# Kernel optimization log

Hardware: AMD Instinct MI355X
Metric: run time of the kernel (lower is better)

Reference implementation:

```python
import jax, jax.numpy as jnp
import numpy as np

DIM = 64

def conv2d_g2(x, w, b):
    # 3x3 conv, padding=1, groups=2, NCHW
    y = jax.lax.conv_general_dilated(x, w, (1, 1), [(1, 1), (1, 1)],
                                     dimension_numbers=('NCHW', 'OIHW', 'NCHW'),
                                     feature_group_count=2)
    return y + b[None, :, None, None]

def bilinear_gather(x, py, px):
    # x: [B,C,H,W]; py,px: [B,K,H,W] float sample coords -> [B,K,H,W,C]
    B, C, H, W = x.shape
    y0 = jnp.floor(py); x0 = jnp.floor(px)
    ly = py - y0; lx = px - x0
    hy = 1.0 - ly; hx = 1.0 - lx
    b_idx = jnp.arange(B)[:, None, None, None]
    def gather(yi, xi):
        valid = (yi >= 0) & (yi < H) & (xi >= 0) & (xi < W)
        yc = jnp.clip(yi, 0, H - 1).astype(jnp.int32)
        xc = jnp.clip(xi, 0, W - 1).astype(jnp.int32)
        v = x[b_idx, :, yc, xc]  # [B,K,H,W,C]
        return v * valid[..., None].astype(x.dtype)
    return (gather(y0, x0) * (hy * hx)[..., None]
            + gather(y0, x0 + 1) * (hy * lx)[..., None]
            + gather(y0 + 1, x0) * (ly * hx)[..., None]
            + gather(y0 + 1, x0 + 1) * (ly * lx)[..., None])

def deform_dw(x, offset, w, b, k, pad, dil):
    # depthwise (groups=C, offset_groups=1) deformable conv, stride 1
    B, C, H, W = x.shape
    K = k * k
    off = offset.reshape(B, K, 2, H, W)  # torchvision layout: (dy,dx) per kernel tap
    ky = jnp.repeat(jnp.arange(k), k).astype(x.dtype)   # [K]
    kx = jnp.tile(jnp.arange(k), k).astype(x.dtype)     # [K]
    base_y = jnp.arange(H, dtype=x.dtype)[None, None, :, None] - pad + dil * ky[None, :, None, None]
    base_x = jnp.arange(W, dtype=x.dtype)[None, None, None, :] - pad + dil * kx[None, :, None, None]
    py = base_y + off[:, :, 0]  # [B,K,H,W]
    px = base_x + off[:, :, 1]
    val = bilinear_gather(x, py, px)  # [B,K,H,W,C]
    return jnp.einsum('bkhwc,ck->bchw', val, w.reshape(C, K)) + b[None, :, None, None]

def lsk_forward(x, w_off3, b_off3, w_off2, b_off2, w7, b7, w5, b5):
    B, C, H, W = x.shape
    offset3 = conv2d_g2(x, w_off3, b_off3)            # [B,98,H,W]
    out1 = deform_dw(x, offset3, w7, b7, 7, 9, 3)     # [B,C,H,W]
    offset2 = conv2d_g2(x, w_off2, b_off2)            # [B,50,H,W]
    out2 = deform_dw(out1, offset2, w5, b5, 5, 6, 3)  # [B,C,H,W]
    feats = jnp.stack([out1, out2], axis=1)           # [B,2,C,H,W]
    gap = feats.mean(axis=(3, 4), keepdims=True)      # [B,2,C,1,1]
    attn = jax.nn.softmax(gap, axis=1)
    return jnp.sum(feats * attn, axis=1)              # [B,C,H,W]

def setup_inputs() -> dict:
    key = jax.random.key(0)
    ks = jax.random.split(key, 9)
    B, C, H, W = 4, DIM, 56, 56
    return {
        'x':      jax.random.normal(ks[0], (B, C, H, W), jnp.float32),
        'w_off3': jax.random.normal(ks[1], (98, C // 2, 3, 3), jnp.float32) * 0.05,
        'b_off3': jax.random.normal(ks[2], (98,), jnp.float32) * 0.05,
        'w_off2': jax.random.normal(ks[3], (50, C // 2, 3, 3), jnp.float32) * 0.05,
        'b_off2': jax.random.normal(ks[4], (50,), jnp.float32) * 0.05,
        'w7':     jax.random.normal(ks[5], (C, 1, 7, 7), jnp.float32) * 0.1,
        'b7':     jax.random.normal(ks[6], (C,), jnp.float32) * 0.05,
        'w5':     jax.random.normal(ks[7], (C, 1, 5, 5), jnp.float32) * 0.1,
        'b5':     jax.random.normal(ks[8], (C,), jnp.float32) * 0.05,
    }

def reference(x, w_off3, b_off3, w_off2, b_off2, w7, b7, w5, b5):
    return lsk_forward(x, w_off3, b_off3, w_off2, b_off2, w7, b7, w5, b5)
```

## Files before the change

kernel.cpp:

```cpp
#include <hip/hip_runtime.h>
#include <hip/hip_fp16.h>
#include <math.h>

#define HH 56
#define WW 56
#define CC 64
#define BB 4
#define HWA (HH*WW)

typedef _Float16 half8_t __attribute__((ext_vector_type(8)));
typedef _Float16 h2_t   __attribute__((ext_vector_type(2)));
typedef float f32x4_t __attribute__((ext_vector_type(4)));

#define PROWS 57
#define PSTRB (PROWS*57*64*4)
#define ROWSTRB (57*64*4)

__global__ __launch_bounds__(256)
void k_prep(const float* __restrict__ x,
            const float* __restrict__ w3, const float* __restrict__ w2,
            const float* __restrict__ b3, const float* __restrict__ b2,
            __half2* __restrict__ xp, _Float16* __restrict__ xh,
            _Float16* __restrict__ Wp, float* __restrict__ bbp) {
    int blk = blockIdx.x;
    int tid = threadIdx.x;
    if (blk < BB*56) {
        __shared__ float ld[64*57];
        int b = blk / 56, y = blk % 56;
        for (int i = tid; i < 64*56; i += 256) {
            int c = i / 56, col = i % 56;
            ld[c*57 + col] = x[((size_t)b*CC + c)*HWA + y*WW + col];
        }
        __syncthreads();
        for (int i = tid; i < 57*64; i += 256) {
            int j = i >> 6, c = i & 63;
            float lo = (j > 0)  ? ld[c*57 + j - 1] : 0.f;
            float hi = (j < 56) ? ld[c*57 + j]     : 0.f;
            xp[((size_t)(b*PROWS + y)*57 + j)*CC + c] = __floats2half2_rn(lo, hi);
        }
        _Float16* dst = xh + (((size_t)(b*2)*56 + y)*58)*32;
#pragma unroll
        for (int g = 0; g < 2; ++g) {
            for (int i = tid; i < 1856; i += 256) {
                int col = i >> 5, ic = i & 31;
                float v = (col >= 1 && col <= 56) ? ld[(g*32 + ic)*57 + col - 1] : 0.f;
                dst[(size_t)g*(56*58*32) + i] = (_Float16)v;
            }
        }
    } else {
        int i = (blk - BB*56)*256 + tid;
        if (i < 46080) {
            int j    = i & 7;
            int lane = (i >> 3) & 63;
            int mt   = (i >> 9) % 5;
            int kt   = (i / 2560) % 9;
            int g    = i / 23040;
            int m  = mt*16 + (lane & 15);
            int ic = (lane >> 4)*8 + j;
            int ky = kt/3, kx = kt%3;
            float v = 0.f;
            if (m < 49)      v = w3[((g*49 + m)*32 + ic)*9 + ky*3 + kx];
            else if (m < 74) v = w2[((g*25 + (m-49))*32 + ic)*9 + ky*3 + kx];
            Wp[i] = (_Float16)v;
        } else if (i < 46240) {
            int t = i - 46080; int g = t/80, m = t%80;
            float v = 0.f;
            if (m < 49)      v = b3[g*49 + m];
            else if (m < 74) v = b2[g*25 + (m-49)];
            bbp[t] = v;
        }
    }
}

__global__ __launch_bounds__(256)
void k_convmfma(const _Float16* __restrict__ xh, const _Float16* __restrict__ Wp,
                const float* __restrict__ bb,
                float* __restrict__ off3, float* __restrict__ off2) {
    __shared__ _Float16 tile[4][3*18*32];
    int blk = blockIdx.x;
    int iy = blk % 56;
    int g  = (blk / 56) & 1;
    int b  = blk / 112;
    int wv   = threadIdx.y;
    int lane = threadIdx.x;
    int n0 = wv * 16;

    const uint4* xs4 = (const uint4*)xh;
    uint4* tl4 = (uint4*)&tile[wv][0];
#pragma unroll
    for (int i = 0; i < 4; ++i) {
        int idx4 = i*64 + lane;
        if (idx4 < 216) {
            int ic4 = idx4 & 3;
            int seg = idx4 >> 2;
            int cl = seg % 18, r = seg / 18;
            int y = iy - 1 + r, col = n0 + cl;
            uint4 v = {0u, 0u, 0u, 0u};
            if (y >= 0 && y < 56 && col < 58)
                v = xs4[((((size_t)(b*2+g)*56 + y)*58 + col) << 2) + ic4];
            tl4[idx4] = v;
        }
    }
    __syncthreads();

    int nlo = lane & 15, khi = lane >> 4;
    f32x4_t acc[5];
#pragma unroll
    for (int mt = 0; mt < 5; ++mt) acc[mt] = (f32x4_t){0.f,0.f,0.f,0.f};

    const half8_t* wp8 = (const half8_t*)Wp;
#pragma unroll
    for (int kt = 0; kt < 9; ++kt) {
        int ky = kt/3, kx = kt%3;
        half8_t bfrag = *(const half8_t*)&tile[wv][((ky*18) + nlo + kx)*32 + khi*8];
#pragma unroll
        for (int mt = 0; mt < 5; ++mt) {
            half8_t afrag = wp8[(((size_t)g*9 + kt)*5 + mt)*64 + lane];
            acc[mt] = __builtin_amdgcn_mfma_f32_16x16x32_f16(afrag, bfrag, acc[mt], 0, 0, 0);
        }
    }

    int pixcol = n0 + nlo;
    if (pixcol < 56) {
        int pix = iy*WW + pixcol;
#pragma unroll
        for (int mt = 0; mt < 5; ++mt) {
#pragma unroll
            for (int r = 0; r < 4; ++r) {
                int m = mt*16 + khi*4 + r;
                if (m < 74) {
                    float val = acc[mt][r] + bb[g*80 + m];
                    if (m < 49)
                        off3[((size_t)b*98 + g*49 + m)*HWA + pix] = val;
                    else
                        off2[((size_t)b*50 + g*25 + (m-49))*HWA + pix] = val;
                }
            }
        }
    }
}

template<int K, int KS, int PAD, bool WP>
__global__ __launch_bounds__(256)
void k_deform(const _Float16* __restrict__ xp, const float* __restrict__ off,
              const float* __restrict__ wg, const float* __restrict__ bias,
              float* __restrict__ out, float* __restrict__ partial,
              _Float16* __restrict__ xpo) {
    __shared__ float lwf[K*64];
    __shared__ float loffs[2*K][9];
    __shared__ float red[8][64];
    int tid = threadIdx.x + threadIdx.y*64;
    int blk = blockIdx.x;
    int xcd = blk & 7;
    int idx = blk >> 3;
    int b   = xcd >> 1;
    int hw0 = (xcd & 1)*(HWA/2) + idx*8;

    for (int i = tid; i < K*64; i += 256) {
        int cch = i / K, t = i % K;
        lwf[t*64 + cch] = wg[i];
    }
    for (int i = tid; i < 4*K; i += 256) {
        int row = i >> 1, half = i & 1;
        float4 v = *(const float4*)&off[((size_t)b*2*K + row)*HWA + hw0 + half*4];
        loffs[row][half*4 + 0] = v.x; loffs[row][half*4 + 1] = v.y;
        loffs[row][half*4 + 2] = v.z; loffs[row][half*4 + 3] = v.w;
    }
    __syncthreads();

    int yp = threadIdx.y;
    int c  = threadIdx.x;

    int mx0 = 0, wz0 = 0, ww0 = 0;
    int mx1 = 0, wz1 = 0, ww1 = 0;
    if (c < K) {
        int t = c;
        int ky = t / KS, kx = t % KS;
#pragma unroll
        for (int s = 0; s < 2; ++s) {
            int p = yp + 4*s;
            int hw = hw0 + p;
            int h = hw / WW, w = hw % WW;
            float py = (float)(h - PAD + 3*ky) + loffs[2*t][p];
            float px = (float)(w - PAD + 3*kx) + loffs[2*t+1][p];
            float y0f = floorf(py), x0f = floorf(px);
            float ly = py - y0f, lx = px - x0f;
            float hy = 1.f - ly, hx = 1.f - lx;
            int y0 = (int)y0f, x0 = (int)x0f;
            int j = x0 + 1;
            bool jv = (j >= 0) && (j <= 56);
            int jc = jv ? j : 0;
            float s0 = ((y0   >= 0) && (y0   < HH) && jv) ? hy : 0.f;
            float s1 = ((y0+1 >= 0) && (y0+1 < HH) && jv) ? ly : 0.f;
            bool use1 = (s0 == 0.f);
            int rbase = use1 ? min(max(y0 + 1, 0), 55) : y0;
            float aw = use1 ? s1 : s0;
            float bw = use1 ? 0.f : s1;
            int mxv = (rbase*57 + jc)*(64*4);
            __half2 wah = __floats2half2_rn(aw*hx, aw*lx);
            __half2 wbh = __floats2half2_rn(bw*hx, bw*lx);
            if (s == 0) { mx0 = mxv; wz0 = *(int*)&wah; ww0 = *(int*)&wbh; }
            else        { mx1 = mxv; wz1 = *(int*)&wah; ww1 = *(int*)&wbh; }
        }
    }

    int grp = c >> 4, li = c & 15;
    int voffb = (grp & 1) * ROWSTRB + li * 16;
    bool pix1 = (grp & 2) != 0;
    bool rowB = (grp & 1) != 0;
    const char* xb = (const char*)xp + (size_t)b*PSTRB;

    f32x4_t acc = (f32x4_t){0.f, 0.f, 0.f, 0.f};
#pragma unroll 8
    for (int t = 0; t < K; ++t) {
        int m0 = (int)__builtin_amdgcn_readlane(mx0, t);
        int m1 = (int)__builtin_amdgcn_readlane(mx1, t);
        int z0 = (int)__builtin_amdgcn_readlane(wz0, t);
        int w0 = (int)__builtin_amdgcn_readlane(ww0, t);
        int z1 = (int)__builtin_amdgcn_readlane(wz1, t);
        int w1 = (int)__builtin_amdgcn_readlane(ww1, t);
        int msel = pix1 ? m1 : m0;
        int wsel = pix1 ? (rowB ? w1 : z1) : (rowB ? w0 : z0);
        uint4 d = *(const uint4*)(xb + msel + voffb);
        float4 lv = *(const float4*)&lwf[t*64 + 4*li];
        h2_t wh = *(h2_t*)&wsel;
        acc[0] = fmaf(__builtin_amdgcn_fdot2(*(h2_t*)&d.x, wh, 0.f, false), lv.x, acc[0]);
        acc[1] = fmaf(__builtin_amdgcn_fdot2(*(h2_t*)&d.y, wh, 0.f, false), lv.y, acc[1]);
        acc[2] = fmaf(__builtin_amdgcn_fdot2(*(h2_t*)&d.z, wh, 0.f, false), lv.z, acc[2]);
        acc[3] = fmaf(__builtin_amdgcn_fdot2(*(h2_t*)&d.w, wh, 0.f, false), lv.w, acc[3]);
    }

    float4 bs4 = *(const float4*)&bias[4*li];
    float o0 = acc[0] + __shfl_xor(acc[0], 16) + bs4.x;
    float o1 = acc[1] + __shfl_xor(acc[1], 16) + bs4.y;
    float o2 = acc[2] + __shfl_xor(acc[2], 16) + bs4.z;
    float o3 = acc[3] + __shfl_xor(acc[3], 16) + bs4.w;

    int hwA = hw0 + yp, hwB = hw0 + yp + 4;
    if (grp == 0) {
        float4 o = {o0, o1, o2, o3};
        *(float4*)&red[yp][4*li] = o;
        *(float4*)&out[((size_t)b*HWA + hwA)*CC + 4*li] = o;
    } else if (grp == 2) {
        float4 o = {o0, o1, o2, o3};
        *(float4*)&red[yp + 4][4*li] = o;
        *(float4*)&out[((size_t)b*HWA + hwB)*CC + 4*li] = o;
    }
    __syncthreads();

    if (WP) {
        float val0 = red[yp][c];
        float val1 = red[yp + 4][c];
#pragma unroll
        for (int s = 0; s < 2; ++s) {
            int hw = s ? hwB : hwA;
            float val = s ? val1 : val0;
            int y = hw / WW, w = hw % WW;
            _Float16* base = xpo + ((size_t)(b*PROWS + y)*57)*CC*2;
            _Float16 hv = (_Float16)val;
            base[((w    )*64 + c)*2 + 1] = hv;
            base[((w + 1)*64 + c)*2 + 0] = hv;
            if (w == 0)  base[(c)*2 + 0] = (_Float16)0.f;
            if (w == 55) base[((56)*64 + c)*2 + 1] = (_Float16)0.f;
        }
    }

    if (yp == 0) {
        float s = red[0][c] + red[1][c] + red[2][c] + red[3][c]
                + red[4][c] + red[5][c] + red[6][c] + red[7][c];
        partial[((size_t)b*(HWA/8) + (hw0 >> 3))*64 + c] = s;
    }
}

__global__ void k_gapA(const float* __restrict__ p1, const float* __restrict__ p2,
                       float* __restrict__ g2) {
    __shared__ float red[4][64];
    int blk = blockIdx.x;
    int chunk = blk % 14;
    int bf    = blk / 14;
    int b     = bf >> 1;
    const float* p = (bf & 1) ? p2 : p1;
    int tid = threadIdx.x;
    int c = tid & 63, s = tid >> 6;
    float sum = 0.f;
#pragma unroll
    for (int i = 0; i < 7; ++i) {
        int j = chunk*28 + s + 4*i;
        sum += p[((size_t)b*(HWA/8) + j)*64 + c];
    }
    red[s][c] = sum;
    __syncthreads();
    if (s == 0)
        g2[((size_t)bf*14 + chunk)*64 + c]
            = red[0][c] + red[1][c] + red[2][c] + red[3][c];
}

__global__ void k_combine16(const float* __restrict__ o1, const float* __restrict__ o2,
                            const float* __restrict__ g2, float* __restrict__ out) {
    __shared__ float ash[128];
    __shared__ float tile[16][65];
    int blk = blockIdx.x;
    int tid = threadIdx.x;
    int b  = blk / 196;
    int t0 = (blk % 196) * 16;

    if (tid < 64) {
        float s1 = 0.f, s2 = 0.f;
#pragma unroll
        for (int k = 0; k < 14; ++k) {
            s1 += g2[((size_t)(b*2+0)*14 + k)*64 + tid];
            s2 += g2[((size_t)(b*2+1)*14 + k)*64 + tid];
        }
        s1 *= (1.f/HWA); s2 *= (1.f/HWA);
        float m  = fmaxf(s1, s2);
        float e1 = expf(s1 - m), e2 = expf(s2 - m);
        float a1 = e1 / (e1 + e2);
        ash[tid]      = a1;
        ash[64 + tid] = 1.f - a1;
    }
    __syncthreads();

    int p  = tid >> 4, c4 = tid & 15;
    size_t idx4 = ((size_t)b*HWA + t0 + p)*16 + c4;
    float4 v1 = ((const float4*)o1)[idx4];
    float4 v2 = ((const float4*)o2)[idx4];
    tile[p][c4*4 + 0] = v1.x*ash[c4*4+0] + v2.x*ash[64+c4*4+0];
    tile[p][c4*4 + 1] = v1.y*ash[c4*4+1] + v2.y*ash[64+c4*4+1];
    tile[p][c4*4 + 2] = v1.z*ash[c4*4+2] + v2.z*ash[64+c4*4+2];
    tile[p][c4*4 + 3] = v1.w*ash[c4*4+3] + v2.w*ash[64+c4*4+3];
    __syncthreads();

    int px = tid & 15, c0 = tid >> 4;
#pragma unroll
    for (int i = 0; i < 4; ++i) {
        int c = c0 + 16*i;
        out[((size_t)b*CC + c)*HWA + t0 + px] = tile[px][c];
    }
}

extern "C" void kernel_launch(void* const* d_in, const int* in_sizes, int n_in,
                              void* d_out, int out_size, void* d_ws, size_t ws_size,
                              hipStream_t stream) {
    const float* x      = (const float*)d_in[0];
    const float* w_off3 = (const float*)d_in[1];
    const float* b_off3 = (const float*)d_in[2];
    const float* w_off2 = (const float*)d_in[3];
    const float* b_off2 = (const float*)d_in[4];
    const float* w7     = (const float*)d_in[5];
    const float* b7     = (const float*)d_in[6];
    const float* w5     = (const float*)d_in[7];
    const float* b5     = (const float*)d_in[8];
    float* out = (float*)d_out;

    const size_t PAIRF = (size_t)BB*PROWS*57*64;
    float* ws    = (float*)d_ws;
    float* off3r = ws;
    float* off2r = off3r + 1229312;
    float* out1  = off2r + 627200;
    float* out2  = out1  + 802816;
    float* xp1f  = out2  + 802816;
    float* xp2f  = xp1f  + PAIRF;
    float* xhf   = xp2f  + PAIRF;
    float* part1 = xhf   + 415744;
    float* part2 = part1 + 100352;
    float* gpA   = part2 + 100352;
    float* wpf   = gpA   + 7168;
    float* bbp   = wpf   + 23040;
    __half2*  xp1  = (__half2*)xp1f;
    _Float16* xp2h = (_Float16*)xp2f;
    _Float16* xh   = (_Float16*)xhf;
    _Float16* Wp   = (_Float16*)wpf;
    size_t need = (size_t)(1229312 + 627200 + 802816*2 + 831744*2 + 415744
                           + 100352*2 + 7168 + 23040 + 160) * 4;
    if (ws_size < need) return;

    k_prep<<<BB*56 + 181, 256, 0, stream>>>(x, w_off3, w_off2, b_off3, b_off2,
                                            xp1, xh, Wp, bbp);
    k_convmfma<<<BB*2*56, dim3(64,4), 0, stream>>>(xh, Wp, bbp, off3r, off2r);
    k_deform<49,7,9,true><<<BB*(HWA/8), dim3(64,4), 0, stream>>>(
        (const _Float16*)xp1, off3r, w7, b7, out1, part1, xp2h);
    k_deform<25,5,6,false><<<BB*(HWA/8), dim3(64,4), 0, stream>>>(
        xp2h, off2r, w5, b5, out2, part2, nullptr);
    k_gapA<<<8*14, 256, 0, stream>>>(part1, part2, gpA);
    k_combine16<<<BB*196, 256, 0, stream>>>(out1, out2, gpA, out);
}
```

Before: 143.1 us.

## Shrink deform blocks to 4 pixels, one thread per channel, atomic GAP reduction

The deform kernel now uses 128-thread blocks covering 4 pixels instead of 256-thread blocks covering 8. Each lane owns one channel and gathers half2 pairs from both rows itself, rather than splitting rows and channel quads across lane groups and combining them with a shuffle. The separate partial-sum GAP kernel is removed: each block atomically adds its channel sums into a small zeroed buffer that combine reads directly. This doubles the number of blocks and cuts launch count by one. In exchange it uses narrower 4-byte gathers, repeats per-block weight staging twice as often, and adds atomics plus a memset.

```diff
diff --git a/kernel.cpp b/kernel.cpp
--- a/kernel.cpp
+++ b/kernel.cpp
@@ -140,31 +140,27 @@
     }
 }
 
-template<int K, int KS, int PAD, bool WP>
-__global__ __launch_bounds__(256)
+template<int K, int KS, int PAD, bool WP, int FL>
+__global__ __launch_bounds__(128)
 void k_deform(const _Float16* __restrict__ xp, const float* __restrict__ off,
               const float* __restrict__ wg, const float* __restrict__ bias,
-              float* __restrict__ out, float* __restrict__ partial,
+              float* __restrict__ out, float* __restrict__ gpA2,
               _Float16* __restrict__ xpo) {
-    __shared__ float lwf[K*64];
-    __shared__ float loffs[2*K][9];
-    __shared__ float red[8][64];
+    __shared__ float lw[K*64];
+    __shared__ float loffs[2*K][4];
+    __shared__ float red[4][64];
     int tid = threadIdx.x + threadIdx.y*64;
     int blk = blockIdx.x;
     int xcd = blk & 7;
     int idx = blk >> 3;
     int b   = xcd >> 1;
-    int hw0 = (xcd & 1)*(HWA/2) + idx*8;
-
-    for (int i = tid; i < K*64; i += 256) {
-        int cch = i / K, t = i % K;
-        lwf[t*64 + cch] = wg[i];
-    }
-    for (int i = tid; i < 4*K; i += 256) {
-        int row = i >> 1, half = i & 1;
-        float4 v = *(const float4*)&off[((size_t)b*2*K + row)*HWA + hw0 + half*4];
-        loffs[row][half*4 + 0] = v.x; loffs[row][half*4 + 1] = v.y;
-        loffs[row][half*4 + 2] = v.z; loffs[row][half*4 + 3] = v.w;
+    int hw0 = (xcd & 1)*(HWA/2) + idx*4;
+
+    for (int i = tid; i < K*64; i += 128)
+        lw[i] = wg[i];
+    for (int i = tid; i < 2*K; i += 128) {
+        float4 v = *(const float4*)&off[((size_t)b*2*K + i)*HWA + hw0];
+        *(float4*)&loffs[i][0] = v;
     }
     __syncthreads();
 
@@ -178,7 +174,7 @@
         int ky = t / KS, kx = t % KS;
 #pragma unroll
         for (int s = 0; s < 2; ++s) {
-            int p = yp + 4*s;
+            int p = yp + 2*s;
             int hw = hw0 + p;
             int h = hw / WW, w = hw % WW;
             float py = (float)(h - PAD + 3*ky) + loffs[2*t][p];
@@ -204,53 +200,36 @@
         }
     }
 
-    int grp = c >> 4, li = c & 15;
-    int voffb = (grp & 1) * ROWSTRB + li * 16;
-    bool pix1 = (grp & 2) != 0;
-    bool rowB = (grp & 1) != 0;
-    const char* xb = (const char*)xp + (size_t)b*PSTRB;
-
-    f32x4_t acc = (f32x4_t){0.f, 0.f, 0.f, 0.f};
+    const char* xc = (const char*)xp + (size_t)b*PSTRB + c*4;
+    float acc0 = 0.f, acc1 = 0.f;
 #pragma unroll 8
     for (int t = 0; t < K; ++t) {
         int m0 = (int)__builtin_amdgcn_readlane(mx0, t);
-        int m1 = (int)__builtin_amdgcn_readlane(mx1, t);
         int z0 = (int)__builtin_amdgcn_readlane(wz0, t);
         int w0 = (int)__builtin_amdgcn_readlane(ww0, t);
+        int m1 = (int)__builtin_amdgcn_readlane(mx1, t);
         int z1 = (int)__builtin_amdgcn_readlane(wz1, t);
         int w1 = (int)__builtin_amdgcn_readlane(ww1, t);
-        int msel = pix1 ? m1 : m0;
-        int wsel = pix1 ? (rowB ? w1 : z1) : (rowB ? w0 : z0);
-        uint4 d = *(const uint4*)(xb + msel + voffb);
-        float4 lv = *(const float4*)&lwf[t*64 + 4*li];
-        h2_t wh = *(h2_t*)&wsel;
-        acc[0] = fmaf(__builtin_amdgcn_fdot2(*(h2_t*)&d.x, wh, 0.f, false), lv.x, acc[0]);
-        acc[1] = fmaf(__builtin_amdgcn_fdot2(*(h2_t*)&d.y, wh, 0.f, false), lv.y, acc[1]);
-        acc[2] = fmaf(__builtin_amdgcn_fdot2(*(h2_t*)&d.z, wh, 0.f, false), lv.z, acc[2]);
-        acc[3] = fmaf(__builtin_amdgcn_fdot2(*(h2_t*)&d.w, wh, 0.f, false), lv.w, acc[3]);
-    }
-
-    float4 bs4 = *(const float4*)&bias[4*li];
-    float o0 = acc[0] + __shfl_xor(acc[0], 16) + bs4.x;
-    float o1 = acc[1] + __shfl_xor(acc[1], 16) + bs4.y;
-    float o2 = acc[2] + __shfl_xor(acc[2], 16) + bs4.z;
-    float o3 = acc[3] + __shfl_xor(acc[3], 16) + bs4.w;
-
-    int hwA = hw0 + yp, hwB = hw0 + yp + 4;
-    if (grp == 0) {
-        float4 o = {o0, o1, o2, o3};
-        *(float4*)&red[yp][4*li] = o;
-        *(float4*)&out[((size_t)b*HWA + hwA)*CC + 4*li] = o;
-    } else if (grp == 2) {
-        float4 o = {o0, o1, o2, o3};
-        *(float4*)&red[yp + 4][4*li] = o;
-        *(float4*)&out[((size_t)b*HWA + hwB)*CC + 4*li] = o;
-    }
-    __syncthreads();
+        h2_t r0a = *(const h2_t*)(xc + m0);
+        h2_t r1a = *(const h2_t*)(xc + m0 + ROWSTRB);
+        h2_t r0b = *(const h2_t*)(xc + m1);
+        h2_t r1b = *(const h2_t*)(xc + m1 + ROWSTRB);
+        float lwv = lw[c*K + t];
+        float v0 = __builtin_amdgcn_fdot2(r0a, *(h2_t*)&z0, 0.f, false);
+        v0 = __builtin_amdgcn_fdot2(r1a, *(h2_t*)&w0, v0, false);
+        float v1 = __builtin_amdgcn_fdot2(r0b, *(h2_t*)&z1, 0.f, false);
+        v1 = __builtin_amdgcn_fdot2(r1b, *(h2_t*)&w1, v1, false);
+        acc0 = fmaf(v0, lwv, acc0);
+        acc1 = fmaf(v1, lwv, acc1);
+    }
+    float bs = bias[c];
+    float val0 = acc0 + bs;
+    float val1 = acc1 + bs;
+    int hwA = hw0 + yp, hwB = hw0 + yp + 2;
+    out[((size_t)b*HWA + hwA)*CC + c] = val0;
+    out[((size_t)b*HWA + hwB)*CC + c] = val1;
 
     if (WP) {
-        float val0 = red[yp][c];
-        float val1 = red[yp + 4][c];
 #pragma unroll
         for (int s = 0; s < 2; ++s) {
             int hw = s ? hwB : hwA;
@@ -265,34 +244,13 @@
         }
     }
 
-    if (yp == 0) {
-        float s = red[0][c] + red[1][c] + red[2][c] + red[3][c]
-                + red[4][c] + red[5][c] + red[6][c] + red[7][c];
-        partial[((size_t)b*(HWA/8) + (hw0 >> 3))*64 + c] = s;
-    }
-}
-
-__global__ void k_gapA(const float* __restrict__ p1, const float* __restrict__ p2,
-                       float* __restrict__ g2) {
-    __shared__ float red[4][64];
-    int blk = blockIdx.x;
-    int chunk = blk % 14;
-    int bf    = blk / 14;
-    int b     = bf >> 1;
-    const float* p = (bf & 1) ? p2 : p1;
-    int tid = threadIdx.x;
-    int c = tid & 63, s = tid >> 6;
-    float sum = 0.f;
-#pragma unroll
-    for (int i = 0; i < 7; ++i) {
-        int j = chunk*28 + s + 4*i;
-        sum += p[((size_t)b*(HWA/8) + j)*64 + c];
-    }
-    red[s][c] = sum;
-    __syncthreads();
-    if (s == 0)
-        g2[((size_t)bf*14 + chunk)*64 + c]
-            = red[0][c] + red[1][c] + red[2][c] + red[3][c];
+    red[yp][c] = val0;
+    red[yp + 2][c] = val1;
+    __syncthreads();
+    if (tid < 64) {
+        float s = red[0][tid] + red[1][tid] + red[2][tid] + red[3][tid];
+        atomicAdd(&gpA2[(b*2 + FL)*64 + tid], s);
+    }
 }
 
 __global__ void k_combine16(const float* __restrict__ o1, const float* __restrict__ o2,
@@ -305,13 +263,8 @@
     int t0 = (blk % 196) * 16;
 
     if (tid < 64) {
-        float s1 = 0.f, s2 = 0.f;
-#pragma unroll
-        for (int k = 0; k < 14; ++k) {
-            s1 += g2[((size_t)(b*2+0)*14 + k)*64 + tid];
-            s2 += g2[((size_t)(b*2+1)*14 + k)*64 + tid];
-        }
-        s1 *= (1.f/HWA); s2 *= (1.f/HWA);
+        float s1 = g2[(size_t)(b*2+0)*64 + tid] * (1.f/HWA);
+        float s2 = g2[(size_t)(b*2+1)*64 + tid] * (1.f/HWA);
         float m  = fmaxf(s1, s2);
         float e1 = expf(s1 - m), e2 = expf(s2 - m);
         float a1 = e1 / (e1 + e2);
@@ -361,26 +314,25 @@
     float* xp1f  = out2  + 802816;
     float* xp2f  = xp1f  + PAIRF;
     float* xhf   = xp2f  + PAIRF;
-    float* part1 = xhf   + 415744;
-    float* part2 = part1 + 100352;
-    float* gpA   = part2 + 100352;
-    float* wpf   = gpA   + 7168;
+    float* gpA   = xhf   + 415744;
+    float* wpf   = gpA   + 512;
     float* bbp   = wpf   + 23040;
     __half2*  xp1  = (__half2*)xp1f;
     _Float16* xp2h = (_Float16*)xp2f;
     _Float16* xh   = (_Float16*)xhf;
     _Float16* Wp   = (_Float16*)wpf;
     size_t need = (size_t)(1229312 + 627200 + 802816*2 + 831744*2 + 415744
-                           + 100352*2 + 7168 + 23040 + 160) * 4;
+                           + 512 + 23040 + 160) * 4;
     if (ws_size < need) return;
+
+    hipMemsetAsync(gpA, 0, 8*64*sizeof(float), stream);
 
     k_prep<<<BB*56 + 181, 256, 0, stream>>>(x, w_off3, w_off2, b_off3, b_off2,
                                             xp1, xh, Wp, bbp);
     k_convmfma<<<BB*2*56, dim3(64,4), 0, stream>>>(xh, Wp, bbp, off3r, off2r);
-    k_deform<49,7,9,true><<<BB*(HWA/8), dim3(64,4), 0, stream>>>(
-        (const _Float16*)xp1, off3r, w7, b7, out1, part1, xp2h);
-    k_deform<25,5,6,false><<<BB*(HWA/8), dim3(64,4), 0, stream>>>(
-        xp2h, off2r, w5, b5, out2, part2, nullptr);
-    k_gapA<<<8*14, 256, 0, stream>>>(part1, part2, gpA);
+    k_deform<49,7,9,true,0><<<BB*(HWA/4), dim3(64,2), 0, stream>>>(
+        (const _Float16*)xp1, off3r, w7, b7, out1, gpA, xp2h);
+    k_deform<25,5,6,false,1><<<BB*(HWA/4), dim3(64,2), 0, stream>>>(
+        xp2h, off2r, w5, b5, out2, gpA, nullptr);
     k_combine16<<<BB*196, 256, 0, stream>>>(out1, out2, gpA, out);
 }
```

Result: slower. 157.6 us (+10.2%).
